# Optimization experiments

Measured on AMD Instinct MI355X. Metric: run time of the kernel, lower is better.

Reference implementation:

```python
import jax, jax.numpy as jnp
import numpy as np

B, S, D, H, HD, FF, W = 2, 4096, 2048, 16, 128, 8192, 256
EPS = 1e-6
ROPE_BASE = 10000.0


def rmsnorm(x, w):
    return x * jax.lax.rsqrt(jnp.mean(x * x, axis=-1, keepdims=True) + EPS) * w


def apply_rope(x):
    # x: [B, H, S, hd]
    hd = x.shape[-1]
    inv = 1.0 / (ROPE_BASE ** (jnp.arange(0, hd, 2, dtype=jnp.float32) / hd))
    ang = jnp.arange(x.shape[2], dtype=jnp.float32)[:, None] * inv[None, :]  # [S, hd/2]
    cos, sin = jnp.cos(ang), jnp.sin(ang)
    x1, x2 = jnp.split(x, 2, axis=-1)
    return jnp.concatenate([x1 * cos - x2 * sin, x1 * sin + x2 * cos], axis=-1)


def setup_inputs() -> dict:
    key = jax.random.key(0)
    ks = jax.random.split(key, 12)
    sc = 0.02
    return {
        "x": jax.random.normal(ks[0], (B, S, D), jnp.float32),
        "Wq": jax.random.normal(ks[1], (D, D), jnp.float32) * sc,
        "Wk": jax.random.normal(ks[2], (D, D), jnp.float32) * sc,
        "Wv": jax.random.normal(ks[3], (D, D), jnp.float32) * sc,
        "Wo": jax.random.normal(ks[4], (D, D), jnp.float32) * sc,
        "qn_w": jnp.ones((HD,), jnp.float32),
        "kn_w": jnp.ones((HD,), jnp.float32),
        "sink_logit": jax.random.normal(ks[5], (H,), jnp.float32) * sc,
        "attn_norm_w": jnp.ones((D,), jnp.float32),
        "ffn_norm_w": jnp.ones((D,), jnp.float32),
        "Wg": jax.random.normal(ks[6], (D, FF), jnp.float32) * sc,
        "Wu": jax.random.normal(ks[7], (D, FF), jnp.float32) * sc,
        "Wd": jax.random.normal(ks[8], (FF, D), jnp.float32) * sc,
    }


def reference(x, Wq, Wk, Wv, Wo, qn_w, kn_w, sink_logit, attn_norm_w, ffn_norm_w, Wg, Wu, Wd):
    # ---- sliding-window attention sublayer ----
    h = rmsnorm(x, attn_norm_w)
    q = (h @ Wq).reshape(B, S, H, HD)
    k = (h @ Wk).reshape(B, S, H, HD)
    v = (h @ Wv).reshape(B, S, H, HD)
    q = rmsnorm(q, qn_w)
    k = rmsnorm(k, kn_w)
    q = apply_rope(q.transpose(0, 2, 1, 3))  # [B,H,S,hd]
    k = apply_rope(k.transpose(0, 2, 1, 3))
    v = v.transpose(0, 2, 1, 3)

    nb = S // W
    qb = q.reshape(B, H, nb, W, HD)
    kb = k.reshape(B, H, nb, W, HD)
    vb = v.reshape(B, H, nb, W, HD)
    # each query block attends to previous block + own block (window=W causal)
    kprev = jnp.concatenate([jnp.zeros_like(kb[:, :, :1]), kb[:, :, :-1]], axis=2)
    vprev = jnp.concatenate([jnp.zeros_like(vb[:, :, :1]), vb[:, :, :-1]], axis=2)
    kl = jnp.concatenate([kprev, kb], axis=3)  # [B,H,nb,2W,hd]
    vl = jnp.concatenate([vprev, vb], axis=3)

    qi = jnp.arange(W)
    kj = jnp.arange(2 * W)
    rel = W + qi[:, None] - kj[None, :]  # q_pos - kv_pos within block pair
    base = (rel >= 0) & (rel < W)  # causal + in-window, [W, 2W]
    blk = jnp.arange(nb)
    kv_pos_valid = (blk[:, None, None] * W - W + kj[None, None, :]) >= 0  # [nb,1,2W]
    mask = base[None, :, :] & kv_pos_valid  # [nb, W, 2W]

    scale = 1.0 / jnp.sqrt(jnp.float32(HD))
    scores = jnp.einsum("bhnqd,bhnkd->bhnqk", qb, kl) * scale
    scores = jnp.where(mask[None, None], scores, jnp.float32(-1e30))
    # attention sink: virtual kv slot 0 with per-head logit, zero value
    sink = jnp.broadcast_to(sink_logit.reshape(1, H, 1, 1, 1), scores.shape[:-1] + (1,))
    logits = jnp.concatenate([sink, scores], axis=-1)
    p = jax.nn.softmax(logits, axis=-1)
    out = jnp.einsum("bhnqk,bhnkd->bhnqd", p[..., 1:], vl)  # sink contributes 0
    out = out.reshape(B, H, S, HD).transpose(0, 2, 1, 3).reshape(B, S, D)
    x = x + out @ Wo

    # ---- SwiGLU FFN sublayer ----
    h2 = rmsnorm(x, ffn_norm_w)
    x = x + (jax.nn.silu(h2 @ Wg) * (h2 @ Wu)) @ Wd
    return x
```

## Files before the change

### kernel.cpp

```cpp
#include <hip/hip_runtime.h>
#include <hip/hip_bf16.h>
#include <stdint.h>

typedef __bf16 bf16_t;
typedef __bf16 bf16x8 __attribute__((ext_vector_type(8)));
typedef float f32x4 __attribute__((ext_vector_type(4)));

#define B_ 2
#define S_ 4096
#define D_ 2048
#define H_ 16
#define HD_ 128
#define FF_ 8192
#define W_ 256
#define NB_ 16
#define ROWS_ 8192

#define BAR() asm volatile("s_barrier" ::: "memory")

__device__ __forceinline__ bool det_bf16(const uint32_t* det) {
  return (det[0] & 0xFFFFu) == 0x3F80u;
}
__device__ __forceinline__ float ldS(const void* p, size_t i, bool isbf) {
  return isbf ? (float)((const bf16_t*)p)[i] : ((const float*)p)[i];
}
__device__ __forceinline__ void ld8(const void* p, size_t i, bool isbf,
                                    float* f) {
  if (isbf) {
    bf16x8 v = *(const bf16x8*)((const bf16_t*)p + i);
#pragma unroll
    for (int j = 0; j < 8; ++j) f[j] = (float)v[j];
  } else {
    const float* s = (const float*)p + i;
    float4 a = *(const float4*)s;
    float4 b = *(const float4*)(s + 4);
    f[0] = a.x; f[1] = a.y; f[2] = a.z; f[3] = a.w;
    f[4] = b.x; f[5] = b.y; f[6] = b.z; f[7] = b.w;
  }
}

__device__ __forceinline__ void gld_lds16(const bf16_t* g, bf16_t* l) {
  __builtin_amdgcn_global_load_lds(
      (const __attribute__((address_space(1))) uint32_t*)g,
      (__attribute__((address_space(3))) uint32_t*)l, 16, 0, 0);
}

__global__ __launch_bounds__(256)
void transpose_k(const void* __restrict__ src, bf16_t* __restrict__ dst,
                 int R, int C, const uint32_t* __restrict__ det) {
  __shared__ __align__(16) bf16_t tile[64][72];
  const bool isbf = det_bf16(det);
  const int nbc = C >> 6;
  const int br = blockIdx.x / nbc, bc = blockIdx.x % nbc;
  const int t = threadIdx.x;
#pragma unroll
  for (int rnd = 0; rnd < 2; ++rnd) {
    int chunk = t + rnd * 256;
    int r = chunk >> 3;
    int c8 = (chunk & 7) << 3;
    float f[8];
    ld8(src, (size_t)(br * 64 + r) * C + bc * 64 + c8, isbf, f);
    union { bf16_t e[8]; int4 v; } u;
#pragma unroll
    for (int j = 0; j < 8; ++j) u.e[j] = (bf16_t)f[j];
    *(int4*)&tile[r][c8] = u.v;
  }
  __syncthreads();
#pragma unroll
  for (int rnd = 0; rnd < 2; ++rnd) {
    int chunk = t + rnd * 256;
    int cc = chunk >> 3;
    int r8 = (chunk & 7) << 3;
    union { bf16_t e[8]; int4 v; } u;
#pragma unroll
    for (int j = 0; j < 8; ++j) u.e[j] = tile[r8 + j][cc];
    *(int4*)&dst[(size_t)(bc * 64 + cc) * R + br * 64 + r8] = u.v;
  }
}

__global__ __launch_bounds__(256)
void rmsnorm_in_k(const void* __restrict__ x, const void* __restrict__ w,
                  bf16_t* __restrict__ out, const uint32_t* __restrict__ det) {
  __shared__ float sm[4];
  const bool isbf = det_bf16(det);
  const size_t row = blockIdx.x;
  const int i0 = threadIdx.x << 3;
  float f[8], ss = 0.f;
  ld8(x, row * D_ + i0, isbf, f);
#pragma unroll
  for (int j = 0; j < 8; ++j) ss += f[j] * f[j];
#pragma unroll
  for (int off = 1; off < 64; off <<= 1) ss += __shfl_xor(ss, off, 64);
  if ((threadIdx.x & 63) == 0) sm[threadIdx.x >> 6] = ss;
  __syncthreads();
  float tot = sm[0] + sm[1] + sm[2] + sm[3];
  float rs = rsqrtf(tot * (1.0f / D_) + 1e-6f);
  float wf[8];
  ld8(w, i0, isbf, wf);
  bf16x8 res;
#pragma unroll
  for (int j = 0; j < 8; ++j) res[j] = (bf16_t)(f[j] * rs * wf[j]);
  *(bf16x8*)&out[row * D_ + i0] = res;
}

__global__ __launch_bounds__(256)
void rmsnorm_f32_k(const float* __restrict__ x, const void* __restrict__ w,
                   bf16_t* __restrict__ out, const uint32_t* __restrict__ det) {
  __shared__ float sm[4];
  const bool isbf = det_bf16(det);
  const size_t row = blockIdx.x;
  const int i0 = threadIdx.x << 3;
  float4 a = *(const float4*)&x[row * D_ + i0];
  float4 b = *(const float4*)&x[row * D_ + i0 + 4];
  float f[8] = {a.x, a.y, a.z, a.w, b.x, b.y, b.z, b.w};
  float ss = 0.f;
#pragma unroll
  for (int j = 0; j < 8; ++j) ss += f[j] * f[j];
#pragma unroll
  for (int off = 1; off < 64; off <<= 1) ss += __shfl_xor(ss, off, 64);
  if ((threadIdx.x & 63) == 0) sm[threadIdx.x >> 6] = ss;
  __syncthreads();
  float tot = sm[0] + sm[1] + sm[2] + sm[3];
  float rs = rsqrtf(tot * (1.0f / D_) + 1e-6f);
  float wf[8];
  ld8(w, i0, isbf, wf);
  bf16x8 res;
#pragma unroll
  for (int j = 0; j < 8; ++j) res[j] = (bf16_t)(f[j] * rs * wf[j]);
  *(bf16x8*)&out[row * D_ + i0] = res;
}

__global__ __launch_bounds__(256)
void qknorm_rope_k(bf16_t* __restrict__ q, bf16_t* __restrict__ k,
                   const void* __restrict__ qw, const void* __restrict__ kw,
                   const uint32_t* __restrict__ det) {
  const bool isbf = det_bf16(det);
  const int wv = threadIdx.x >> 6;
  const int i = threadIdx.x & 63;
  const int idx = blockIdx.x * 4 + wv;
  const int s = (idx >> 4) & (S_ - 1);
  const size_t base = (size_t)idx * HD_;

  float inv = exp2f((float)i * -0.20762050593046014f);
  float ang = (float)s * inv;
  float sn, cs;
  sincosf(ang, &sn, &cs);

#pragma unroll
  for (int t = 0; t < 2; ++t) {
    bf16_t* p = (t == 0) ? (q + base) : (k + base);
    const void* w = (t == 0) ? qw : kw;
    float x1 = (float)p[i], x2 = (float)p[i + 64];
    float ss = x1 * x1 + x2 * x2;
#pragma unroll
    for (int off = 1; off < 64; off <<= 1) ss += __shfl_xor(ss, off, 64);
    float rs = rsqrtf(ss * (1.0f / HD_) + 1e-6f);
    float n1 = x1 * rs * ldS(w, i, isbf);
    float n2 = x2 * rs * ldS(w, i + 64, isbf);
    p[i] = (bf16_t)(n1 * cs - n2 * sn);
    p[i + 64] = (bf16_t)(n1 * sn + n2 * cs);
  }
}

#define TQ 8192

template <int EPI>
__global__ __launch_bounds__(512, 2)
void gemm256_k(const bf16_t* __restrict__ A, const bf16_t* __restrict__ Bt,
               void* __restrict__ C, const void* __restrict__ aux,
               const uint32_t* __restrict__ det, int M, int N, int K) {
  extern __shared__ __align__(16) bf16_t lds[];
  bf16_t* Ab = lds;
  bf16_t* Bb = lds + 4 * TQ;

  bool isbf = false;
  if constexpr (EPI == 1 || EPI == 3) isbf = det_bf16(det);

  const int tid = threadIdx.x;
  const int lane = tid & 63, wid = tid >> 6;
  const int l15 = lane & 15, l4 = lane >> 4;
  const int wm = wid >> 2, wn = wid & 3;

  const int nwg = gridDim.x;
  const int nbm = M >> 8;
  const int orig = blockIdx.x;
  const int q8 = nwg >> 3, r8 = nwg & 7, xcd = orig & 7;
  const int swz = (xcd < r8 ? xcd * (q8 + 1) : r8 * (q8 + 1) + (xcd - r8) * q8)
                + (orig >> 3);
  const int bm = swz % nbm;
  const int bn = swz / nbm;

  const bf16_t* Ag = A + (size_t)(bm * 256) * K;
  const bf16_t* Bg = Bt + (size_t)(bn * 256) * K;

  const int c0 = tid, c1 = 512 + tid;
  const int r0 = c0 >> 2, r1 = c1 >> 2;
  const size_t goff0 = (size_t)r0 * K + (((c0 & 3) ^ ((r0 >> 1) & 3)) << 3);
  const size_t goff1 = (size_t)r1 * K + (((c1 & 3) ^ ((r1 >> 1) & 3)) << 3);
  const int loff0 = c0 * 8, loff1 = c1 * 8;

  int aoff[8], boff[4];
#pragma unroll
  for (int m = 0; m < 8; ++m) {
    int R = wm * 128 + m * 16 + l15;
    aoff[m] = R * 32 + ((l4 ^ ((R >> 1) & 3)) << 3);
  }
#pragma unroll
  for (int n = 0; n < 4; ++n) {
    int R = wn * 64 + n * 16 + l15;
    boff[n] = R * 32 + ((l4 ^ ((R >> 1) & 3)) << 3);
  }

  f32x4 acc[8][4] = {};
  const int nt = K >> 5;

  gld_lds16(Ag + goff0, Ab + loff0);
  gld_lds16(Ag + goff1, Ab + loff1);
  gld_lds16(Bg + goff0, Bb + loff0);
  gld_lds16(Bg + goff1, Bb + loff1);
  gld_lds16(Ag + 32 + goff0, Ab + TQ + loff0);
  gld_lds16(Ag + 32 + goff1, Ab + TQ + loff1);
  gld_lds16(Bg + 32 + goff0, Bb + TQ + loff0);
  gld_lds16(Bg + 32 + goff1, Bb + TQ + loff1);
  asm volatile("s_waitcnt vmcnt(4)" ::: "memory");
  BAR();

  for (int t = 0; t < nt; ++t) {
    const bf16_t* a = Ab + (t & 3) * TQ;
    const bf16_t* b = Bb + (t & 3) * TQ;

    bf16x8 af[8], bfr[4];
#pragma unroll
    for (int n = 0; n < 4; ++n) bfr[n] = *(const bf16x8*)&b[boff[n]];
#pragma unroll
    for (int m = 0; m < 8; ++m) af[m] = *(const bf16x8*)&a[aoff[m]];

    if (t + 2 < nt) {
      bf16_t* la = Ab + ((t + 2) & 3) * TQ;
      bf16_t* lb = Bb + ((t + 2) & 3) * TQ;
      const size_t k0 = (size_t)(t + 2) << 5;
      gld_lds16(Ag + k0 + goff0, la + loff0);
      gld_lds16(Ag + k0 + goff1, la + loff1);
      gld_lds16(Bg + k0 + goff0, lb + loff0);
      gld_lds16(Bg + k0 + goff1, lb + loff1);
    }

#pragma unroll
    for (int m = 0; m < 8; ++m)
#pragma unroll
      for (int n = 0; n < 4; ++n)
        acc[m][n] = __builtin_amdgcn_mfma_f32_16x16x32_bf16(af[m], bfr[n],
                                                            acc[m][n], 0, 0, 0);

    if (t + 2 < nt) { asm volatile("s_waitcnt vmcnt(4)" ::: "memory"); }
    else            { asm volatile("s_waitcnt vmcnt(0)" ::: "memory"); }
    BAR();
  }

#pragma unroll
  for (int m8 = 0; m8 < 8; ++m8) {
#pragma unroll
    for (int r = 0; r < 4; ++r) {
      const int row = bm * 256 + wm * 128 + m8 * 16 + l4 * 4 + r;
#pragma unroll
      for (int n = 0; n < 4; ++n) {
        const int col = bn * 256 + wn * 64 + n * 16 + l15;
        const size_t idx = (size_t)row * N + col;
        const float val = acc[m8][n][r];
        if constexpr (EPI == 0) {
          ((bf16_t*)C)[idx] = (bf16_t)val;
        } else if constexpr (EPI == 1) {
          ((float*)C)[idx] = ldS(aux, idx, isbf) + val;
        } else if constexpr (EPI == 2) {
          float g = (float)((const bf16_t*)aux)[idx];
          float sg = g / (1.f + __expf(-g));
          ((bf16_t*)C)[idx] = (bf16_t)(sg * val);
        } else {
          float v = ((const float*)aux)[idx] + val;
          if (isbf) ((bf16_t*)C)[idx] = (bf16_t)v;
          else      ((float*)C)[idx] = v;
        }
      }
    }
  }
}

__global__ __launch_bounds__(512)
void attn_k(const bf16_t* __restrict__ Q, const bf16_t* __restrict__ K,
            const bf16_t* __restrict__ V, const void* __restrict__ sink,
            bf16_t* __restrict__ O, const uint32_t* __restrict__ det) {
  __shared__ __align__(16) bf16_t Ks[64][128];
  __shared__ __align__(16) bf16_t Vt[128][64];
  __shared__ __align__(16) bf16_t Ps[8][32][64];

  const bool isbf = det_bf16(det);
  const int bx = blockIdx.x;
  const int n = bx & (NB_ - 1);
  const int h = (bx >> 4) & (H_ - 1);
  const int b = bx >> 8;
  const int tid = threadIdx.x;
  const int wv = tid >> 6, lane = tid & 63;
  const int l15 = lane & 15, l4 = lane >> 4;
  const size_t headbase = ((size_t)b * S_ * H_ + h) * HD_;
  const int RS = H_ * HD_;
  const int q0 = n * W_;
  const int wq = wv * 32;

  bf16x8 qf[2][4];
#pragma unroll
  for (int mi = 0; mi < 2; ++mi)
#pragma unroll
    for (int kb = 0; kb < 4; ++kb) {
      int s = q0 + wq + mi * 16 + l15;
      qf[mi][kb] = *(const bf16x8*)&Q[headbase + (size_t)s * RS + kb * 32 + l4 * 8];
    }

  const float sinkl = ldS(sink, h, isbf);
  float m_run[2][4], l_run[2][4];
#pragma unroll
  for (int mi = 0; mi < 2; ++mi)
#pragma unroll
    for (int r = 0; r < 4; ++r) { m_run[mi][r] = sinkl; l_run[mi][r] = 1.0f; }
  f32x4 oacc[2][8] = {};

  const int kvbase = q0 - W_;
  const float scale = 0.088388347648318447f;

  for (int c = 0; c < 8; ++c) {
    __syncthreads();
#pragma unroll
    for (int rnd = 0; rnd < 2; ++rnd) {
      int chunk = tid + rnd * 512;
      int r = chunk >> 4;
      int c8 = (chunk & 15) << 3;
      int sk = kvbase + c * 64 + r;
      int4 kv = {0, 0, 0, 0}, vvv = {0, 0, 0, 0};
      if (sk >= 0) {
        kv = *(const int4*)&K[headbase + (size_t)sk * RS + c8];
        vvv = *(const int4*)&V[headbase + (size_t)sk * RS + c8];
      }
      *(int4*)&Ks[r][c8] = kv;
      const bf16_t* pv = (const bf16_t*)&vvv;
#pragma unroll
      for (int j = 0; j < 8; ++j) Vt[c8 + j][r] = pv[j];
    }
    __syncthreads();

    bool any = (c * 64 + 63 >= wq + 1) && (c * 64 <= wq + 31 + W_);
    if (n == 0 && c < 4) any = false;
    if (!any) continue;

    f32x4 sacc[2][4] = {};
#pragma unroll
    for (int kb = 0; kb < 4; ++kb) {
      bf16x8 kf[4];
#pragma unroll
      for (int ni = 0; ni < 4; ++ni)
        kf[ni] = *(const bf16x8*)&Ks[ni * 16 + l15][kb * 32 + l4 * 8];
#pragma unroll
      for (int mi = 0; mi < 2; ++mi)
#pragma unroll
        for (int ni = 0; ni < 4; ++ni)
          sacc[mi][ni] = __builtin_amdgcn_mfma_f32_16x16x32_bf16(
              qf[mi][kb], kf[ni], sacc[mi][ni], 0, 0, 0);
    }

#pragma unroll
    for (int mi = 0; mi < 2; ++mi) {
#pragma unroll
      for (int r = 0; r < 4; ++r) {
        const int qi = wq + mi * 16 + l4 * 4 + r;
        float mx = -3.0e38f;
#pragma unroll
        for (int ni = 0; ni < 4; ++ni) {
          int kj = c * 64 + ni * 16 + l15;
          bool ok = (kj > qi) && (kj <= qi + W_) && (n > 0 || kj >= W_);
          float sv = ok ? sacc[mi][ni][r] * scale : -1.0e30f;
          sacc[mi][ni][r] = sv;
          mx = fmaxf(mx, sv);
        }
#pragma unroll
        for (int off = 1; off < 16; off <<= 1)
          mx = fmaxf(mx, __shfl_xor(mx, off, 64));
        float mo = m_run[mi][r];
        float mn = fmaxf(mo, mx);
        float alpha = __expf(mo - mn);
        m_run[mi][r] = mn;
        float rs = 0.f;
#pragma unroll
        for (int ni = 0; ni < 4; ++ni) {
          float p = __expf(sacc[mi][ni][r] - mn);
          sacc[mi][ni][r] = p;
          rs += p;
        }
#pragma unroll
        for (int off = 1; off < 16; off <<= 1) rs += __shfl_xor(rs, off, 64);
        l_run[mi][r] = l_run[mi][r] * alpha + rs;
#pragma unroll
        for (int ni = 0; ni < 8; ++ni) oacc[mi][ni][r] *= alpha;
      }
    }

#pragma unroll
    for (int mi = 0; mi < 2; ++mi)
#pragma unroll
      for (int ni = 0; ni < 4; ++ni)
#pragma unroll
        for (int r = 0; r < 4; ++r)
          Ps[wv][mi * 16 + l4 * 4 + r][ni * 16 + l15] = (bf16_t)sacc[mi][ni][r];

#pragma unroll
    for (int kb2 = 0; kb2 < 2; ++kb2) {
      bf16x8 pf[2];
#pragma unroll
      for (int mi = 0; mi < 2; ++mi)
        pf[mi] = *(const bf16x8*)&Ps[wv][mi * 16 + l15][kb2 * 32 + l4 * 8];
#pragma unroll
      for (int ni = 0; ni < 8; ++ni) {
        bf16x8 vf = *(const bf16x8*)&Vt[ni * 16 + l15][kb2 * 32 + l4 * 8];
#pragma unroll
        for (int mi = 0; mi < 2; ++mi)
          oacc[mi][ni] = __builtin_amdgcn_mfma_f32_16x16x32_bf16(
              pf[mi], vf, oacc[mi][ni], 0, 0, 0);
      }
    }
  }

#pragma unroll
  for (int mi = 0; mi < 2; ++mi)
#pragma unroll
    for (int r = 0; r < 4; ++r) {
      float inv = 1.0f / l_run[mi][r];
      int s = q0 + wq + mi * 16 + l4 * 4 + r;
#pragma unroll
      for (int ni = 0; ni < 8; ++ni)
        O[headbase + (size_t)s * RS + ni * 16 + l15] =
            (bf16_t)(oacc[mi][ni][r] * inv);
    }
}

extern "C" void kernel_launch(void* const* d_in, const int* in_sizes, int n_in,
                              void* d_out, int out_size, void* d_ws,
                              size_t ws_size, hipStream_t stream) {
  const void* x   = d_in[0];
  const void* Wq  = d_in[1];
  const void* Wk  = d_in[2];
  const void* Wv  = d_in[3];
  const void* Wo  = d_in[4];
  const void* qnw = d_in[5];
  const void* knw = d_in[6];
  const void* snk = d_in[7];
  const void* anw = d_in[8];
  const void* fnw = d_in[9];
  const void* Wg  = d_in[10];
  const void* Wu  = d_in[11];
  const void* Wd  = d_in[12];
  const uint32_t* det = (const uint32_t*)anw;

  char* ws = (char*)d_ws;
  const size_t MB = 1024ull * 1024ull;
  bf16_t* WT = (bf16_t*)(ws + 0 * MB);
  bf16_t* hb = (bf16_t*)(ws + 32 * MB);
  bf16_t* qb = (bf16_t*)(ws + 64 * MB);
  bf16_t* kb = (bf16_t*)(ws + 96 * MB);
  bf16_t* vb = (bf16_t*)(ws + 128 * MB);
  bf16_t* ao = (bf16_t*)(ws + 160 * MB);
  float* xm  = (float*)(ws + 192 * MB);
  bf16_t* gb = (bf16_t*)(ws + 64 * MB);

  const int LDSZ = 131072;
  hipFuncSetAttribute((const void*)gemm256_k<0>,
                      hipFuncAttributeMaxDynamicSharedMemorySize, LDSZ);
  hipFuncSetAttribute((const void*)gemm256_k<1>,
                      hipFuncAttributeMaxDynamicSharedMemorySize, LDSZ);
  hipFuncSetAttribute((const void*)gemm256_k<2>,
                      hipFuncAttributeMaxDynamicSharedMemorySize, LDSZ);
  hipFuncSetAttribute((const void*)gemm256_k<3>,
                      hipFuncAttributeMaxDynamicSharedMemorySize, LDSZ);

  rmsnorm_in_k<<<ROWS_, 256, 0, stream>>>(x, anw, hb, det);

  transpose_k<<<32 * 32, 256, 0, stream>>>(Wq, WT, 2048, 2048, det);
  gemm256_k<0><<<32 * 8, 512, LDSZ, stream>>>(hb, WT, qb, nullptr, det, 8192, 2048, 2048);
  transpose_k<<<32 * 32, 256, 0, stream>>>(Wk, WT, 2048, 2048, det);
  gemm256_k<0><<<32 * 8, 512, LDSZ, stream>>>(hb, WT, kb, nullptr, det, 8192, 2048, 2048);
  transpose_k<<<32 * 32, 256, 0, stream>>>(Wv, WT, 2048, 2048, det);
  gemm256_k<0><<<32 * 8, 512, LDSZ, stream>>>(hb, WT, vb, nullptr, det, 8192, 2048, 2048);

  qknorm_rope_k<<<B_ * S_ * H_ / 4, 256, 0, stream>>>(qb, kb, qnw, knw, det);

  attn_k<<<B_ * H_ * NB_, 512, 0, stream>>>(qb, kb, vb, snk, ao, det);

  transpose_k<<<32 * 32, 256, 0, stream>>>(Wo, WT, 2048, 2048, det);
  gemm256_k<1><<<32 * 8, 512, LDSZ, stream>>>(ao, WT, xm, x, det, 8192, 2048, 2048);

  rmsnorm_f32_k<<<ROWS_, 256, 0, stream>>>(xm, fnw, hb, det);

  transpose_k<<<32 * 128, 256, 0, stream>>>(Wg, WT, 2048, 8192, det);
  gemm256_k<0><<<32 * 32, 512, LDSZ, stream>>>(hb, WT, gb, nullptr, det, 8192, 8192, 2048);
  transpose_k<<<32 * 128, 256, 0, stream>>>(Wu, WT, 2048, 8192, det);
  gemm256_k<2><<<32 * 32, 512, LDSZ, stream>>>(hb, WT, gb, gb, det, 8192, 8192, 2048);
  transpose_k<<<128 * 32, 256, 0, stream>>>(Wd, WT, 8192, 2048, det);
  gemm256_k<3><<<32 * 8, 512, LDSZ, stream>>>(gb, WT, d_out, xm, det, 8192, 2048, 8192);

  (void)in_sizes; (void)n_in; (void)out_size; (void)ws_size;
}
```

Before: 1.376 ms.

## Deepen GEMM global-to-LDS prefetch to three stages and interleave fragment loads

The bf16 MFMA GEMM main loop now keeps three K-tiles in flight in its four-slot LDS ring instead of two. The prefetch for tile t+3 is issued at the top of each iteration, and the vmcnt waits are adjusted to allow eight outstanding loads. A-fragment LDS reads are spread through the MFMA loop, two rows ahead, so LDS latency can overlap with matrix math. The aim is to hide more global memory latency, at the cost of more outstanding loads and more complex wait logic near the loop tail.

```diff
diff --git a/kernel.cpp b/kernel.cpp
--- a/kernel.cpp
+++ b/kernel.cpp
@@ -199,6 +199,16 @@
   const size_t goff1 = (size_t)r1 * K + (((c1 & 3) ^ ((r1 >> 1) & 3)) << 3);
   const int loff0 = c0 * 8, loff1 = c1 * 8;
 
+  auto stage = [&](int tt) {
+    bf16_t* la = Ab + (tt & 3) * TQ;
+    bf16_t* lb = Bb + (tt & 3) * TQ;
+    const size_t k0 = (size_t)tt << 5;
+    gld_lds16(Ag + k0 + goff0, la + loff0);
+    gld_lds16(Ag + k0 + goff1, la + loff1);
+    gld_lds16(Bg + k0 + goff0, lb + loff0);
+    gld_lds16(Bg + k0 + goff1, lb + loff1);
+  };
+
   int aoff[8], boff[4];
 #pragma unroll
   for (int m = 0; m < 8; ++m) {
@@ -214,46 +224,36 @@
   f32x4 acc[8][4] = {};
   const int nt = K >> 5;
 
-  gld_lds16(Ag + goff0, Ab + loff0);
-  gld_lds16(Ag + goff1, Ab + loff1);
-  gld_lds16(Bg + goff0, Bb + loff0);
-  gld_lds16(Bg + goff1, Bb + loff1);
-  gld_lds16(Ag + 32 + goff0, Ab + TQ + loff0);
-  gld_lds16(Ag + 32 + goff1, Ab + TQ + loff1);
-  gld_lds16(Bg + 32 + goff0, Bb + TQ + loff0);
-  gld_lds16(Bg + 32 + goff1, Bb + TQ + loff1);
-  asm volatile("s_waitcnt vmcnt(4)" ::: "memory");
+  stage(0);
+  stage(1);
+  stage(2);
+  asm volatile("s_waitcnt vmcnt(8)" ::: "memory");
   BAR();
 
   for (int t = 0; t < nt; ++t) {
     const bf16_t* a = Ab + (t & 3) * TQ;
     const bf16_t* b = Bb + (t & 3) * TQ;
 
-    bf16x8 af[8], bfr[4];
+    if (t + 3 < nt) stage(t + 3);
+
+    bf16x8 bfr[4], af[8];
 #pragma unroll
     for (int n = 0; n < 4; ++n) bfr[n] = *(const bf16x8*)&b[boff[n]];
-#pragma unroll
-    for (int m = 0; m < 8; ++m) af[m] = *(const bf16x8*)&a[aoff[m]];
-
-    if (t + 2 < nt) {
-      bf16_t* la = Ab + ((t + 2) & 3) * TQ;
-      bf16_t* lb = Bb + ((t + 2) & 3) * TQ;
-      const size_t k0 = (size_t)(t + 2) << 5;
-      gld_lds16(Ag + k0 + goff0, la + loff0);
-      gld_lds16(Ag + k0 + goff1, la + loff1);
-      gld_lds16(Bg + k0 + goff0, lb + loff0);
-      gld_lds16(Bg + k0 + goff1, lb + loff1);
-    }
-
-#pragma unroll
-    for (int m = 0; m < 8; ++m)
+    af[0] = *(const bf16x8*)&a[aoff[0]];
+    af[1] = *(const bf16x8*)&a[aoff[1]];
+
+#pragma unroll
+    for (int m = 0; m < 8; ++m) {
+      if (m + 2 < 8) af[m + 2] = *(const bf16x8*)&a[aoff[m + 2]];
 #pragma unroll
       for (int n = 0; n < 4; ++n)
         acc[m][n] = __builtin_amdgcn_mfma_f32_16x16x32_bf16(af[m], bfr[n],
                                                             acc[m][n], 0, 0, 0);
-
-    if (t + 2 < nt) { asm volatile("s_waitcnt vmcnt(4)" ::: "memory"); }
-    else            { asm volatile("s_waitcnt vmcnt(0)" ::: "memory"); }
+    }
+
+    if (t + 3 < nt)      { asm volatile("s_waitcnt vmcnt(8)" ::: "memory"); }
+    else if (t + 2 < nt) { asm volatile("s_waitcnt vmcnt(4)" ::: "memory"); }
+    else if (t + 1 < nt) { asm volatile("s_waitcnt vmcnt(0)" ::: "memory"); }
     BAR();
   }
 
```

Result: slower. 1.453 ms (+5.6%).

## Fuse Q/K/V projections into one GEMM with interleaved QKV buffer

Applied to the files above, without the earlier changes.

Stacks the transposed Wq, Wk, Wv weights and runs one 8192x6144 GEMM into a packed QKV buffer with row stride 6144, replacing three separate GEMM launches. The rope and attention kernels are updated to read Q, K and V at offsets within that row. The GEMM tile mapping is also changed to group four M-tiles per N-column for better L2 reuse of B tiles. This cuts launch count and tail effects and reuses the A operand across all three projections. The cost is strided rather than contiguous reads in attention, and the new tile order affects every GEMM.

```diff
diff --git a/kernel.cpp b/kernel.cpp
--- a/kernel.cpp
+++ b/kernel.cpp
@@ -15,6 +15,7 @@
 #define W_ 256
 #define NB_ 16
 #define ROWS_ 8192
+#define QS_ 6144
 
 #define BAR() asm volatile("s_barrier" ::: "memory")
 
@@ -131,15 +132,18 @@
 }
 
 __global__ __launch_bounds__(256)
-void qknorm_rope_k(bf16_t* __restrict__ q, bf16_t* __restrict__ k,
-                   const void* __restrict__ qw, const void* __restrict__ kw,
+void qknorm_rope_k(bf16_t* __restrict__ qkv, const void* __restrict__ qw,
+                   const void* __restrict__ kw,
                    const uint32_t* __restrict__ det) {
   const bool isbf = det_bf16(det);
   const int wv = threadIdx.x >> 6;
   const int i = threadIdx.x & 63;
   const int idx = blockIdx.x * 4 + wv;
-  const int s = (idx >> 4) & (S_ - 1);
-  const size_t base = (size_t)idx * HD_;
+  const int row = idx >> 4;
+  const int s = row & (S_ - 1);
+  const int h = idx & 15;
+  bf16_t* qp = qkv + (size_t)row * QS_ + h * HD_;
+  bf16_t* kp = qp + 2048;
 
   float inv = exp2f((float)i * -0.20762050593046014f);
   float ang = (float)s * inv;
@@ -148,7 +152,7 @@
 
 #pragma unroll
   for (int t = 0; t < 2; ++t) {
-    bf16_t* p = (t == 0) ? (q + base) : (k + base);
+    bf16_t* p = (t == 0) ? qp : kp;
     const void* w = (t == 0) ? qw : kw;
     float x1 = (float)p[i], x2 = (float)p[i + 64];
     float ss = x1 * x1 + x2 * x2;
@@ -182,13 +186,15 @@
   const int wm = wid >> 2, wn = wid & 3;
 
   const int nwg = gridDim.x;
-  const int nbm = M >> 8;
+  const int nbn = N >> 8;
   const int orig = blockIdx.x;
   const int q8 = nwg >> 3, r8 = nwg & 7, xcd = orig & 7;
   const int swz = (xcd < r8 ? xcd * (q8 + 1) : r8 * (q8 + 1) + (xcd - r8) * q8)
                 + (orig >> 3);
-  const int bm = swz % nbm;
-  const int bn = swz / nbm;
+  const int grp = swz / (4 * nbn);
+  const int rem = swz % (4 * nbn);
+  const int bm = grp * 4 + (rem & 3);
+  const int bn = rem >> 2;
 
   const bf16_t* Ag = A + (size_t)(bm * 256) * K;
   const bf16_t* Bg = Bt + (size_t)(bn * 256) * K;
@@ -286,8 +292,7 @@
 }
 
 __global__ __launch_bounds__(512)
-void attn_k(const bf16_t* __restrict__ Q, const bf16_t* __restrict__ K,
-            const bf16_t* __restrict__ V, const void* __restrict__ sink,
+void attn_k(const bf16_t* __restrict__ QKV, const void* __restrict__ sink,
             bf16_t* __restrict__ O, const uint32_t* __restrict__ det) {
   __shared__ __align__(16) bf16_t Ks[64][128];
   __shared__ __align__(16) bf16_t Vt[128][64];
@@ -301,8 +306,8 @@
   const int tid = threadIdx.x;
   const int wv = tid >> 6, lane = tid & 63;
   const int l15 = lane & 15, l4 = lane >> 4;
-  const size_t headbase = ((size_t)b * S_ * H_ + h) * HD_;
-  const int RS = H_ * HD_;
+  const size_t qkvbase = (size_t)b * S_ * QS_ + h * HD_;
+  const size_t obase = ((size_t)b * S_ * H_ + h) * HD_;
   const int q0 = n * W_;
   const int wq = wv * 32;
 
@@ -312,7 +317,7 @@
 #pragma unroll
     for (int kb = 0; kb < 4; ++kb) {
       int s = q0 + wq + mi * 16 + l15;
-      qf[mi][kb] = *(const bf16x8*)&Q[headbase + (size_t)s * RS + kb * 32 + l4 * 8];
+      qf[mi][kb] = *(const bf16x8*)&QKV[qkvbase + (size_t)s * QS_ + kb * 32 + l4 * 8];
     }
 
   const float sinkl = ldS(sink, h, isbf);
@@ -336,8 +341,9 @@
       int sk = kvbase + c * 64 + r;
       int4 kv = {0, 0, 0, 0}, vvv = {0, 0, 0, 0};
       if (sk >= 0) {
-        kv = *(const int4*)&K[headbase + (size_t)sk * RS + c8];
-        vvv = *(const int4*)&V[headbase + (size_t)sk * RS + c8];
+        const bf16_t* src = &QKV[qkvbase + (size_t)sk * QS_ + c8];
+        kv = *(const int4*)(src + 2048);
+        vvv = *(const int4*)(src + 4096);
       }
       *(int4*)&Ks[r][c8] = kv;
       const bf16_t* pv = (const bf16_t*)&vvv;
@@ -434,7 +440,7 @@
       int s = q0 + wq + mi * 16 + l4 * 4 + r;
 #pragma unroll
       for (int ni = 0; ni < 8; ++ni)
-        O[headbase + (size_t)s * RS + ni * 16 + l15] =
+        O[obase + (size_t)s * (H_ * HD_) + ni * 16 + l15] =
             (bf16_t)(oacc[mi][ni][r] * inv);
     }
 }
@@ -459,14 +465,12 @@
 
   char* ws = (char*)d_ws;
   const size_t MB = 1024ull * 1024ull;
-  bf16_t* WT = (bf16_t*)(ws + 0 * MB);
-  bf16_t* hb = (bf16_t*)(ws + 32 * MB);
-  bf16_t* qb = (bf16_t*)(ws + 64 * MB);
-  bf16_t* kb = (bf16_t*)(ws + 96 * MB);
-  bf16_t* vb = (bf16_t*)(ws + 128 * MB);
-  bf16_t* ao = (bf16_t*)(ws + 160 * MB);
-  float* xm  = (float*)(ws + 192 * MB);
-  bf16_t* gb = (bf16_t*)(ws + 64 * MB);
+  bf16_t* WT  = (bf16_t*)(ws + 0 * MB);
+  bf16_t* hb  = (bf16_t*)(ws + 32 * MB);
+  bf16_t* qkv = (bf16_t*)(ws + 64 * MB);
+  bf16_t* ao  = (bf16_t*)(ws + 160 * MB);
+  float* xm   = (float*)(ws + 192 * MB);
+  bf16_t* gb  = (bf16_t*)(ws + 64 * MB);
 
   const int LDSZ = 131072;
   hipFuncSetAttribute((const void*)gemm256_k<0>,
@@ -481,15 +485,14 @@
   rmsnorm_in_k<<<ROWS_, 256, 0, stream>>>(x, anw, hb, det);
 
   transpose_k<<<32 * 32, 256, 0, stream>>>(Wq, WT, 2048, 2048, det);
-  gemm256_k<0><<<32 * 8, 512, LDSZ, stream>>>(hb, WT, qb, nullptr, det, 8192, 2048, 2048);
-  transpose_k<<<32 * 32, 256, 0, stream>>>(Wk, WT, 2048, 2048, det);
-  gemm256_k<0><<<32 * 8, 512, LDSZ, stream>>>(hb, WT, kb, nullptr, det, 8192, 2048, 2048);
-  transpose_k<<<32 * 32, 256, 0, stream>>>(Wv, WT, 2048, 2048, det);
-  gemm256_k<0><<<32 * 8, 512, LDSZ, stream>>>(hb, WT, vb, nullptr, det, 8192, 2048, 2048);
-
-  qknorm_rope_k<<<B_ * S_ * H_ / 4, 256, 0, stream>>>(qb, kb, qnw, knw, det);
-
-  attn_k<<<B_ * H_ * NB_, 512, 0, stream>>>(qb, kb, vb, snk, ao, det);
+  transpose_k<<<32 * 32, 256, 0, stream>>>(Wk, WT + 2048 * 2048, 2048, 2048, det);
+  transpose_k<<<32 * 32, 256, 0, stream>>>(Wv, WT + 2 * 2048 * 2048, 2048, 2048, det);
+  gemm256_k<0><<<32 * 24, 512, LDSZ, stream>>>(hb, WT, qkv, nullptr, det,
+                                               8192, 6144, 2048);
+
+  qknorm_rope_k<<<B_ * S_ * H_ / 4, 256, 0, stream>>>(qkv, qnw, knw, det);
+
+  attn_k<<<B_ * H_ * NB_, 512, 0, stream>>>(qkv, snk, ao, det);
 
   transpose_k<<<32 * 32, 256, 0, stream>>>(Wo, WT, 2048, 2048, det);
   gemm256_k<1><<<32 * 8, 512, LDSZ, stream>>>(ao, WT, xm, x, det, 8192, 2048, 2048);
```

New measurement: 1.335 ms. 3.0% less time.
